# Optimization experiments

Measured on AMD Instinct MI355X. Metric: run time of the kernel, lower is better.

## Reference

```python
import jax, jax.numpy as jnp
import numpy as np

N = 50000
NEG_SLOPE = 0.2  # PyG GATConv default


def _add_self_loops(edge_index, n):
    loop = jnp.arange(n, dtype=edge_index.dtype)
    src = jnp.concatenate([edge_index[0], loop])
    dst = jnp.concatenate([edge_index[1], loop])
    return src, dst


def _gat_layer(x, src, dst, W, a_src, a_dst, b, concat):
    n = x.shape[0]
    H, C = a_src.shape
    h = (x @ W).reshape(n, H, C)                      # [N,H,C]
    s_src = jnp.sum(h * a_src, axis=-1)               # [N,H] per-node src score
    s_dst = jnp.sum(h * a_dst, axis=-1)               # [N,H] per-node dst score
    e = jax.nn.leaky_relu(s_src[src] + s_dst[dst], NEG_SLOPE)  # [E,H]
    m = jax.ops.segment_max(e, dst, num_segments=n)   # segment softmax (stable)
    ex = jnp.exp(e - m[dst])
    denom = jax.ops.segment_sum(ex, dst, num_segments=n)
    alpha = ex / denom[dst]                           # [E,H]
    out = jax.ops.segment_sum(h[src] * alpha[:, :, None], dst, num_segments=n)
    out = out.reshape(n, H * C) if concat else out.mean(axis=1)
    return out + b


def setup_inputs() -> dict:
    key = jax.random.key(0)
    ks = jax.random.split(key, 10)
    in_dim, hid, heads1, out_dim, heads2 = 256, 16, 8, 64, 1
    x = jax.random.normal(ks[0], (N, in_dim), dtype=jnp.float32)
    edge_index = jax.random.randint(ks[1], (2, 800000), 0, N, dtype=jnp.int64)
    sc1 = 1.0 / np.sqrt(in_dim)
    sc2 = 1.0 / np.sqrt(hid * heads1)
    W1 = jax.random.normal(ks[2], (in_dim, heads1 * hid), dtype=jnp.float32) * sc1
    a1_src = jax.random.normal(ks[3], (heads1, hid), dtype=jnp.float32) * sc1
    a1_dst = jax.random.normal(ks[4], (heads1, hid), dtype=jnp.float32) * sc1
    b1 = jnp.zeros((heads1 * hid,), dtype=jnp.float32)
    W2 = jax.random.normal(ks[5], (heads1 * hid, heads2 * out_dim), dtype=jnp.float32) * sc2
    a2_src = jax.random.normal(ks[6], (heads2, out_dim), dtype=jnp.float32) * sc2
    a2_dst = jax.random.normal(ks[7], (heads2, out_dim), dtype=jnp.float32) * sc2
    b2 = jnp.zeros((out_dim,), dtype=jnp.float32)
    return {"x": x, "edge_index": edge_index, "W1": W1, "a1_src": a1_src,
            "a1_dst": a1_dst, "b1": b1, "W2": W2, "a2_src": a2_src,
            "a2_dst": a2_dst, "b2": b2}


def reference(x, edge_index, W1, a1_src, a1_dst, b1, W2, a2_src, a2_dst, b2):
    # eval mode: dropout layers are identity
    src, dst = _add_self_loops(edge_index, x.shape[0])
    h = _gat_layer(x, src, dst, W1, a1_src, a1_dst, b1, concat=True)
    h = jax.nn.elu(h)
    out = _gat_layer(h, src, dst, W2, a2_src, a2_dst, b2, concat=False)
    return jax.nn.log_softmax(out, axis=1)
```

## Files before the change

### kernel.cpp

```cpp
#include <hip/hip_runtime.h>
#include <hip/hip_bf16.h>

typedef __attribute__((ext_vector_type(8))) short short8;
typedef __attribute__((ext_vector_type(4))) float f32x4;

#define EDGE_CHUNK 4096

__device__ __forceinline__ float lrelu(float v) { return fmaxf(v, 0.2f * v); }

__device__ __forceinline__ short bf16_hi(float f, float* back) {
    __hip_bfloat16 h = __float2bfloat16(f);
    *back = __bfloat162float(h);
    return __builtin_bit_cast(short, h);
}
__device__ __forceinline__ short f2bf(float f) {
    return __builtin_bit_cast(short, __float2bfloat16(f));
}

__global__ void packWs_kernel(const float* __restrict__ W1, const float* __restrict__ a1s,
                              const float* __restrict__ a1d, const float* __restrict__ W2,
                              const float* __restrict__ a2s, const float* __restrict__ a2d,
                              float* __restrict__ W1sd, float* __restrict__ W2sd) {
    int t = blockIdx.x * blockDim.x + threadIdx.x;
    if (t < 256 * 16) {
        int k = t >> 4, hh = t & 15;
        int h = hh & 7;
        const float* a = (hh >= 8) ? a1d : a1s;
        float s = 0.f;
#pragma unroll
        for (int c = 0; c < 16; c++) s += W1[k * 128 + h * 16 + c] * a[h * 16 + c];
        W1sd[t] = s;
    } else {
        int u = t - 4096;
        if (u < 128 * 2) {
            int k = u >> 1;
            const float* a = (u & 1) ? a2d : a2s;
            float s = 0.f;
#pragma unroll
            for (int c = 0; c < 64; c++) s += W2[k * 64 + c] * a[c];
            W2sd[u] = s;
        }
    }
}

template <int K, int NW, int NSD>
__global__ void packW_kernel(const float* __restrict__ W, const float* __restrict__ Wsd,
                             short* __restrict__ hi, short* __restrict__ lo) {
    constexpr int N = NW + 16;
    constexpr int NT = N / 16;
    int t = blockIdx.x * blockDim.x + threadIdx.x;
    if (t >= K * N) return;
    int j = t & 7, lane = (t >> 3) & 63, tile = t >> 9;
    int nt = tile % NT, kt = tile / NT;
    int k = kt * 32 + (lane >> 4) * 8 + j;
    int c = nt * 16 + (lane & 15);
    float w;
    if (c < NW) w = W[(size_t)k * NW + c];
    else if (c - NW < NSD) w = Wsd[(size_t)k * NSD + (c - NW)];
    else w = 0.f;
    float back;
    hi[t] = bf16_hi(w, &back);
    lo[t] = f2bf(w - back);
}

template <int K, int NT, int MODE>
__launch_bounds__(256)
__global__ void mfma_gemm(const float* __restrict__ A, const short* __restrict__ Bhi,
                          const short* __restrict__ Blo, unsigned short* __restrict__ hb,
                          float* __restrict__ s_s, float* __restrict__ s_d, int M) {
    constexpr int KT = K / 32;
    constexpr int NH = NT - 1;
    const int wave = threadIdx.x >> 6, lane = threadIdx.x & 63;
    const int row0 = (blockIdx.x * 4 + wave) * 16;
    if (row0 >= M) return;
    const int arow = row0 + (lane & 15);
    const float* ap = A + (size_t)arow * K + (lane >> 4) * 8;

    f32x4 acc[NT];
#pragma unroll
    for (int i = 0; i < NT; i++) acc[i] = (f32x4){0.f, 0.f, 0.f, 0.f};

    for (int kt = 0; kt < KT; kt++) {
        float av[8];
        *(float4*)(av)     = *(const float4*)(ap + kt * 32);
        *(float4*)(av + 4) = *(const float4*)(ap + kt * 32 + 4);
        short8 ahi, alo;
#pragma unroll
        for (int j = 0; j < 8; j++) {
            float back;
            ahi[j] = bf16_hi(av[j], &back);
            alo[j] = f2bf(av[j] - back);
        }
        const short8* bh = (const short8*)(Bhi + ((size_t)(kt * NT) * 64 + lane) * 8);
        const short8* bl = (const short8*)(Blo + ((size_t)(kt * NT) * 64 + lane) * 8);
#pragma unroll
        for (int nt = 0; nt < NT; nt++) {
            short8 bhv = bh[nt * 64];
            short8 blv = bl[nt * 64];
            acc[nt] = __builtin_amdgcn_mfma_f32_16x16x32_bf16(ahi, bhv, acc[nt], 0, 0, 0);
            acc[nt] = __builtin_amdgcn_mfma_f32_16x16x32_bf16(ahi, blv, acc[nt], 0, 0, 0);
            acc[nt] = __builtin_amdgcn_mfma_f32_16x16x32_bf16(alo, bhv, acc[nt], 0, 0, 0);
        }
    }
    const int orow0 = row0 + (lane >> 4) * 4;
    const int col = lane & 15;
#pragma unroll
    for (int nt = 0; nt < NH; nt++)
#pragma unroll
        for (int r = 0; r < 4; r++)
            hb[(size_t)(orow0 + r) * (NH * 16) + nt * 16 + col] =
                (unsigned short)f2bf(acc[nt][r]);
#pragma unroll
    for (int r = 0; r < 4; r++) {
        int orow = orow0 + r;
        float v = acc[NH][r];
        if (MODE == 1) {
            if (col < 8) s_s[orow * 8 + col] = v;
            else         s_d[orow * 8 + (col - 8)] = v;
        } else {
            if (col == 0)      s_s[orow] = v;
            else if (col == 1) s_d[orow] = v;
        }
    }
}

__global__ void hist_kernel(const int* __restrict__ ei, int E, int n, int* __restrict__ deg) {
    int slot = blockIdx.x & 7;
    int chunk = blockIdx.x >> 3;
    int lo = (int)(((long)n * slot) >> 3);
    int hi = (int)(((long)n * (slot + 1)) >> 3);
    int ET = E + n;
    int base = chunk * EDGE_CHUNK;
    int endi = min(base + EDGE_CHUNK, ET);
    for (int i = base + threadIdx.x; i < endi; i += 256) {
        int d = (i < E) ? ei[E + i] : i - E;
        if (d >= lo && d < hi) atomicAdd(&deg[d], 1);
    }
}

__global__ void scatter_kernel(const int* __restrict__ ei, int E, int n,
                               int* __restrict__ cursor, int* __restrict__ csr_src) {
    int slot = blockIdx.x & 7;
    int chunk = blockIdx.x >> 3;
    int lo = (int)(((long)n * slot) >> 3);
    int hi = (int)(((long)n * (slot + 1)) >> 3);
    int ET = E + n;
    int base = chunk * EDGE_CHUNK;
    int endi = min(base + EDGE_CHUNK, ET);
    for (int i = base + threadIdx.x; i < endi; i += 256) {
        int s, d;
        if (i < E) { s = ei[i]; d = ei[E + i]; } else { s = d = i - E; }
        if (d >= lo && d < hi) {
            int pos = atomicAdd(&cursor[d], 1);
            csr_src[pos] = s;
        }
    }
}

__global__ void scan_block(const int* __restrict__ deg, int n, int* __restrict__ incl,
                           int* __restrict__ bsum) {
    __shared__ int wsum[16];
    int i = blockIdx.x * 1024 + threadIdx.x;
    int lane = threadIdx.x & 63, wv = threadIdx.x >> 6;
    int v = (i < n) ? deg[i] : 0;
    int s = v;
#pragma unroll
    for (int off = 1; off < 64; off <<= 1) {
        int t = __shfl_up(s, off, 64);
        if (lane >= off) s += t;
    }
    if (lane == 63) wsum[wv] = s;
    __syncthreads();
    if (wv == 0) {
        int w = (lane < 16) ? wsum[lane] : 0;
#pragma unroll
        for (int off = 1; off < 16; off <<= 1) {
            int t = __shfl_up(w, off, 64);
            if (lane >= off) w += t;
        }
        if (lane < 16) wsum[lane] = w;
    }
    __syncthreads();
    int add = wv ? wsum[wv - 1] : 0;
    if (i < n) incl[i] = s + add;
    if (threadIdx.x == 1023) bsum[blockIdx.x] = s + add;
}

__global__ void scan_tops(const int* __restrict__ bsum, int nb, int* __restrict__ boff) {
    int lane = threadIdx.x;
    int v = (lane < nb) ? bsum[lane] : 0;
    int s = v;
#pragma unroll
    for (int off = 1; off < 64; off <<= 1) {
        int t = __shfl_up(s, off, 64);
        if (lane >= off) s += t;
    }
    if (lane < nb) boff[lane] = s - v;
    if (lane == 63) boff[nb] = s;
}

__global__ void scan_final(const int* __restrict__ incl, const int* __restrict__ deg,
                           const int* __restrict__ boff, int n, int nb,
                           int* __restrict__ rowptr, int* __restrict__ cursor) {
    int i = blockIdx.x * 1024 + threadIdx.x;
    if (i < n) {
        int v = boff[i >> 10] + incl[i] - deg[i];
        rowptr[i] = v;
        cursor[i] = v;
    }
    if (i == 0) rowptr[n] = boff[nb];
}

__launch_bounds__(256)
__global__ void gather1_kernel(const int* __restrict__ rowptr, const int* __restrict__ csr_src,
                               const float* __restrict__ ssrc, const float* __restrict__ sdst,
                               const unsigned short* __restrict__ h1b,
                               const float* __restrict__ b1, float* __restrict__ out1, int n) {
    int wid = blockIdx.x * 4 + (threadIdx.x >> 6);
    if (wid >= n) return;
    int lane = threadIdx.x & 63;
    int eg = lane >> 3;
    int hs = lane & 7;
    int ha = lane >> 3;
    float sd_s = sdst[wid * 8 + hs];
    int beg = rowptr[wid], end = rowptr[wid + 1];
    float den_p = 0.f, a0 = 0.f, a1 = 0.f;

    for (int i = beg; i < end; i += 8) {
        int idx = i + eg;
        int src = 0;
        float e = 0.f;
        if (idx < end) {
            src = csr_src[idx];
            e = __expf(lrelu(ssrc[src * 8 + hs] + sd_s));
        }
        den_p += e;
        int nn = end - i;
#define G1_BODY(k)                                                                  \
        {                                                                           \
            float eb = __shfl(e, (k) * 8 + ha, 64);                                 \
            int sb = __shfl(src, (k) * 8, 64);                                      \
            unsigned xw = *(const unsigned*)(h1b + (size_t)sb * 128 + 2 * lane);    \
            a0 = __builtin_fmaf(eb, __uint_as_float(xw << 16), a0);                 \
            a1 = __builtin_fmaf(eb, __uint_as_float(xw & 0xffff0000u), a1);         \
        }
        if (nn >= 8) {
#pragma unroll
            for (int k = 0; k < 8; k++) G1_BODY(k)
        } else {
            for (int k = 0; k < nn; k++) G1_BODY(k)
        }
#undef G1_BODY
    }
    den_p += __shfl_xor(den_p, 8, 64);
    den_p += __shfl_xor(den_p, 16, 64);
    den_p += __shfl_xor(den_p, 32, 64);
    float den = __shfl(den_p, ha, 64);
    float inv = 1.f / den;
    float2 bb = *(const float2*)(b1 + 2 * lane);
    float o0 = __builtin_fmaf(a0, inv, bb.x);
    float o1 = __builtin_fmaf(a1, inv, bb.y);
    float2 o;
    o.x = o0 > 0.f ? o0 : (__expf(o0) - 1.f);
    o.y = o1 > 0.f ? o1 : (__expf(o1) - 1.f);
    *(float2*)(out1 + (size_t)wid * 128 + 2 * lane) = o;
}

__launch_bounds__(256)
__global__ void gather2_kernel(const int* __restrict__ rowptr, const int* __restrict__ csr_src,
                               const float* __restrict__ ssrc, const float* __restrict__ sdst,
                               const unsigned short* __restrict__ h2b,
                               const float* __restrict__ b2, float* __restrict__ out, int n) {
    int wid = blockIdx.x * 4 + (threadIdx.x >> 6);
    if (wid >= n) return;
    int lane = threadIdx.x & 63;
    float sd = sdst[wid];
    int beg = rowptr[wid], end = rowptr[wid + 1];
    float den_p = 0.f, acc = 0.f;

    for (int i = beg; i < end; i += 64) {
        int idx = i + lane;
        int src = 0;
        float e = 0.f;
        if (idx < end) {
            src = csr_src[idx];
            e = __expf(lrelu(ssrc[src] + sd));
        }
        den_p += e;
        int nn = end - i; if (nn > 64) nn = 64;
#define G2_BODY(k)                                                                  \
        {                                                                           \
            float eb = __shfl(e, (k), 64);                                          \
            int sb = __shfl(src, (k), 64);                                          \
            float x = __uint_as_float(((unsigned)h2b[(size_t)sb * 64 + lane]) << 16);\
            acc = __builtin_fmaf(eb, x, acc);                                       \
        }
        int k = 0;
        for (; k + 8 <= nn; k += 8) {
#pragma unroll
            for (int u = 0; u < 8; u++) G2_BODY(k + u)
        }
        for (; k < nn; k++) G2_BODY(k)
#undef G2_BODY
    }
#pragma unroll
    for (int off = 1; off < 64; off <<= 1) den_p += __shfl_xor(den_p, off, 64);

    float o = acc / den_p + b2[lane];
    float mx = o;
#pragma unroll
    for (int off = 32; off; off >>= 1) mx = fmaxf(mx, __shfl_xor(mx, off, 64));
    float ex = __expf(o - mx);
    float sum = ex;
#pragma unroll
    for (int off = 32; off; off >>= 1) sum += __shfl_xor(sum, off, 64);
    out[(size_t)wid * 64 + lane] = o - mx - logf(sum);
}

extern "C" void kernel_launch(void* const* d_in, const int* in_sizes, int n_in,
                              void* d_out, int out_size, void* d_ws, size_t ws_size,
                              hipStream_t stream) {
    const float* x   = (const float*)d_in[0];
    const int*   ei  = (const int*)d_in[1];
    const float* W1  = (const float*)d_in[2];
    const float* a1s = (const float*)d_in[3];
    const float* a1d = (const float*)d_in[4];
    const float* b1  = (const float*)d_in[5];
    const float* W2  = (const float*)d_in[6];
    const float* a2s = (const float*)d_in[7];
    const float* a2d = (const float*)d_in[8];
    const float* b2  = (const float*)d_in[9];
    float* out = (float*)d_out;

    const int n = in_sizes[0] / 256;
    const int E = in_sizes[1] / 2;
    const int ET = E + n;
    const int NB = (n + 1023) / 1024;
    const int NCH = (ET + EDGE_CHUNK - 1) / EDGE_CHUNK;

    float* ws = (float*)d_ws;
    float* out1 = ws;
    float* s1s  = out1 + (size_t)n * 128;
    float* s1d  = s1s + (size_t)n * 8;
    float* s2s  = s1d + (size_t)n * 8;
    float* s2d  = s2s + n;
    unsigned short* h1b = (unsigned short*)(s2d + n);
    unsigned short* h2b = h1b + (size_t)n * 128;
    int*   deg     = (int*)(h2b + (size_t)n * 64);
    int*   rowptr  = deg + n;
    int*   cursor  = rowptr + n + 1;
    int*   csr_src = cursor + n;
    int*   incl    = csr_src + ET;
    int*   bsum    = incl + n;
    int*   boff    = bsum + NB;
    float* W1sd    = (float*)(boff + NB + 1);
    float* W2sd    = W1sd + 256 * 16;
    short* w1hi    = (short*)(W2sd + 128 * 2);
    short* w1lo    = w1hi + 256 * 144;
    short* w2hi    = w1lo + 256 * 144;
    short* w2lo    = w2hi + 128 * 80;

    hipMemsetAsync(deg, 0, (size_t)n * 4, stream);

    const int B = 256;

    packWs_kernel<<<(4096 + 256 + B - 1) / B, B, 0, stream>>>(W1, a1s, a1d, W2, a2s, a2d,
                                                              W1sd, W2sd);
    packW_kernel<256, 128, 16><<<(256 * 144 + B - 1) / B, B, 0, stream>>>(W1, W1sd, w1hi, w1lo);
    packW_kernel<128, 64, 2><<<(128 * 80 + B - 1) / B, B, 0, stream>>>(W2, W2sd, w2hi, w2lo);

    hist_kernel<<<8 * NCH, B, 0, stream>>>(ei, E, n, deg);
    scan_block<<<NB, 1024, 0, stream>>>(deg, n, incl, bsum);
    scan_tops<<<1, 64, 0, stream>>>(bsum, NB, boff);
    scan_final<<<NB, 1024, 0, stream>>>(incl, deg, boff, n, NB, rowptr, cursor);
    scatter_kernel<<<8 * NCH, B, 0, stream>>>(ei, E, n, cursor, csr_src);

    mfma_gemm<256, 9, 1><<<(n + 63) / 64, 256, 0, stream>>>(x, w1hi, w1lo, h1b, s1s, s1d, n);
    gather1_kernel<<<(n + 3) / 4, 256, 0, stream>>>(rowptr, csr_src, s1s, s1d, h1b, b1, out1, n);

    mfma_gemm<128, 5, 2><<<(n + 63) / 64, 256, 0, stream>>>(out1, w2hi, w2lo, h2b, s2s, s2d, n);
    gather2_kernel<<<(n + 3) / 4, 256, 0, stream>>>(rowptr, csr_src, s2s, s2d, h2b, b2, out, n);
}
```

Measured before the change: 314.9 us.

## Merge weight packing kernels and software-pipeline edge index loads in gathers

Folds the attention-vector projection and the bf16 hi/lo weight packing of both layers into a single kernel, cutting two launches and an intermediate buffer. Both gather kernels now prefetch the next chunk's source indices and source scores, loading indices two iterations ahead, so the dependent index-then-score load chain overlaps with the current chunk's feature accumulation. This raises register pressure and adds some redundant bounds-checked loads near the end of each row.

```diff
diff --git a/kernel.cpp b/kernel.cpp
--- a/kernel.cpp
+++ b/kernel.cpp
@@ -17,50 +17,49 @@
     return __builtin_bit_cast(short, __float2bfloat16(f));
 }
 
-__global__ void packWs_kernel(const float* __restrict__ W1, const float* __restrict__ a1s,
-                              const float* __restrict__ a1d, const float* __restrict__ W2,
-                              const float* __restrict__ a2s, const float* __restrict__ a2d,
-                              float* __restrict__ W1sd, float* __restrict__ W2sd) {
+__global__ void packW_all(const float* __restrict__ W1, const float* __restrict__ a1s,
+                          const float* __restrict__ a1d, const float* __restrict__ W2,
+                          const float* __restrict__ a2s, const float* __restrict__ a2d,
+                          short* __restrict__ w1hi, short* __restrict__ w1lo,
+                          short* __restrict__ w2hi, short* __restrict__ w2lo) {
     int t = blockIdx.x * blockDim.x + threadIdx.x;
-    if (t < 256 * 16) {
-        int k = t >> 4, hh = t & 15;
-        int h = hh & 7;
-        const float* a = (hh >= 8) ? a1d : a1s;
-        float s = 0.f;
-#pragma unroll
-        for (int c = 0; c < 16; c++) s += W1[k * 128 + h * 16 + c] * a[h * 16 + c];
-        W1sd[t] = s;
+    if (t < 256 * 144) {
+        int j = t & 7, lane = (t >> 3) & 63, tile = t >> 9;
+        int nt = tile % 9, kt = tile / 9;
+        int k = kt * 32 + (lane >> 4) * 8 + j;
+        int c = nt * 16 + (lane & 15);
+        float w;
+        if (c < 128) {
+            w = W1[(size_t)k * 128 + c];
+        } else {
+            int hh = c - 128, h = hh & 7;
+            const float* a = (hh >= 8) ? a1d : a1s;
+            w = 0.f;
+#pragma unroll
+            for (int q = 0; q < 16; q++) w += W1[(size_t)k * 128 + h * 16 + q] * a[h * 16 + q];
+        }
+        float back;
+        w1hi[t] = bf16_hi(w, &back);
+        w1lo[t] = f2bf(w - back);
     } else {
-        int u = t - 4096;
-        if (u < 128 * 2) {
-            int k = u >> 1;
-            const float* a = (u & 1) ? a2d : a2s;
-            float s = 0.f;
-#pragma unroll
-            for (int c = 0; c < 64; c++) s += W2[k * 64 + c] * a[c];
-            W2sd[u] = s;
-        }
-    }
-}
-
-template <int K, int NW, int NSD>
-__global__ void packW_kernel(const float* __restrict__ W, const float* __restrict__ Wsd,
-                             short* __restrict__ hi, short* __restrict__ lo) {
-    constexpr int N = NW + 16;
-    constexpr int NT = N / 16;
-    int t = blockIdx.x * blockDim.x + threadIdx.x;
-    if (t >= K * N) return;
-    int j = t & 7, lane = (t >> 3) & 63, tile = t >> 9;
-    int nt = tile % NT, kt = tile / NT;
-    int k = kt * 32 + (lane >> 4) * 8 + j;
-    int c = nt * 16 + (lane & 15);
-    float w;
-    if (c < NW) w = W[(size_t)k * NW + c];
-    else if (c - NW < NSD) w = Wsd[(size_t)k * NSD + (c - NW)];
-    else w = 0.f;
-    float back;
-    hi[t] = bf16_hi(w, &back);
-    lo[t] = f2bf(w - back);
+        int u = t - 256 * 144;
+        if (u >= 128 * 80) return;
+        int j = u & 7, lane = (u >> 3) & 63, tile = u >> 9;
+        int nt = tile % 5, kt = tile / 5;
+        int k = kt * 32 + (lane >> 4) * 8 + j;
+        int c = nt * 16 + (lane & 15);
+        float w = 0.f;
+        if (c < 64) {
+            w = W2[(size_t)k * 64 + c];
+        } else if (c < 66) {
+            const float* a = (c == 65) ? a2d : a2s;
+#pragma unroll
+            for (int q = 0; q < 64; q++) w += W2[(size_t)k * 64 + q] * a[q];
+        }
+        float back;
+        w2hi[u] = bf16_hi(w, &back);
+        w2lo[u] = f2bf(w - back);
+    }
 }
 
 template <int K, int NT, int MODE>
@@ -226,20 +225,21 @@
     int beg = rowptr[wid], end = rowptr[wid + 1];
     float den_p = 0.f, a0 = 0.f, a1 = 0.f;
 
+    int idx0 = beg + eg;
+    int src_c = (idx0 < end) ? csr_src[idx0] : 0;
+    int src_n = (idx0 + 8 < end) ? csr_src[idx0 + 8] : 0;
+    float sc_c = (idx0 < end) ? ssrc[src_c * 8 + hs] : 0.f;
+
     for (int i = beg; i < end; i += 8) {
-        int idx = i + eg;
-        int src = 0;
-        float e = 0.f;
-        if (idx < end) {
-            src = csr_src[idx];
-            e = __expf(lrelu(ssrc[src * 8 + hs] + sd_s));
-        }
+        int src_n2 = (i + 16 + eg < end) ? csr_src[i + 16 + eg] : 0;
+        float sc_n = (i + 8 + eg < end) ? ssrc[src_n * 8 + hs] : 0.f;
+        float e = (i + eg < end) ? __expf(lrelu(sc_c + sd_s)) : 0.f;
         den_p += e;
         int nn = end - i;
 #define G1_BODY(k)                                                                  \
         {                                                                           \
             float eb = __shfl(e, (k) * 8 + ha, 64);                                 \
-            int sb = __shfl(src, (k) * 8, 64);                                      \
+            int sb = __shfl(src_c, (k) * 8, 64);                                    \
             unsigned xw = *(const unsigned*)(h1b + (size_t)sb * 128 + 2 * lane);    \
             a0 = __builtin_fmaf(eb, __uint_as_float(xw << 16), a0);                 \
             a1 = __builtin_fmaf(eb, __uint_as_float(xw & 0xffff0000u), a1);         \
@@ -251,6 +251,7 @@
             for (int k = 0; k < nn; k++) G1_BODY(k)
         }
 #undef G1_BODY
+        src_c = src_n; src_n = src_n2; sc_c = sc_n;
     }
     den_p += __shfl_xor(den_p, 8, 64);
     den_p += __shfl_xor(den_p, 16, 64);
@@ -278,20 +279,21 @@
     int beg = rowptr[wid], end = rowptr[wid + 1];
     float den_p = 0.f, acc = 0.f;
 
+    int idx0 = beg + lane;
+    int src_c = (idx0 < end) ? csr_src[idx0] : 0;
+    int src_n = (idx0 + 64 < end) ? csr_src[idx0 + 64] : 0;
+    float sc_c = (idx0 < end) ? ssrc[src_c] : 0.f;
+
     for (int i = beg; i < end; i += 64) {
-        int idx = i + lane;
-        int src = 0;
-        float e = 0.f;
-        if (idx < end) {
-            src = csr_src[idx];
-            e = __expf(lrelu(ssrc[src] + sd));
-        }
+        int src_n2 = (i + 128 + lane < end) ? csr_src[i + 128 + lane] : 0;
+        float sc_n = (i + 64 + lane < end) ? ssrc[src_n] : 0.f;
+        float e = (i + lane < end) ? __expf(lrelu(sc_c + sd)) : 0.f;
         den_p += e;
         int nn = end - i; if (nn > 64) nn = 64;
 #define G2_BODY(k)                                                                  \
         {                                                                           \
             float eb = __shfl(e, (k), 64);                                          \
-            int sb = __shfl(src, (k), 64);                                          \
+            int sb = __shfl(src_c, (k), 64);                                        \
             float x = __uint_as_float(((unsigned)h2b[(size_t)sb * 64 + lane]) << 16);\
             acc = __builtin_fmaf(eb, x, acc);                                       \
         }
@@ -302,6 +304,7 @@
         }
         for (; k < nn; k++) G2_BODY(k)
 #undef G2_BODY
+        src_c = src_n; src_n = src_n2; sc_c = sc_n;
     }
 #pragma unroll
     for (int off = 1; off < 64; off <<= 1) den_p += __shfl_xor(den_p, off, 64);
@@ -353,9 +356,7 @@
     int*   incl    = csr_src + ET;
     int*   bsum    = incl + n;
     int*   boff    = bsum + NB;
-    float* W1sd    = (float*)(boff + NB + 1);
-    float* W2sd    = W1sd + 256 * 16;
-    short* w1hi    = (short*)(W2sd + 128 * 2);
+    short* w1hi    = (short*)(boff + NB + 1);
     short* w1lo    = w1hi + 256 * 144;
     short* w2hi    = w1lo + 256 * 144;
     short* w2lo    = w2hi + 128 * 80;
@@ -364,10 +365,8 @@
 
     const int B = 256;
 
-    packWs_kernel<<<(4096 + 256 + B - 1) / B, B, 0, stream>>>(W1, a1s, a1d, W2, a2s, a2d,
-                                                              W1sd, W2sd);
-    packW_kernel<256, 128, 16><<<(256 * 144 + B - 1) / B, B, 0, stream>>>(W1, W1sd, w1hi, w1lo);
-    packW_kernel<128, 64, 2><<<(128 * 80 + B - 1) / B, B, 0, stream>>>(W2, W2sd, w2hi, w2lo);
+    packW_all<<<(256 * 144 + 128 * 80 + B - 1) / B, B, 0, stream>>>(
+        W1, a1s, a1d, W2, a2s, a2d, w1hi, w1lo, w2hi, w2lo);
 
     hist_kernel<<<8 * NCH, B, 0, stream>>>(ei, E, n, deg);
     scan_block<<<NB, 1024, 0, stream>>>(deg, n, incl, bsum);
```

Result: faster. 303.4 us (-3.6%).
